# Optimization experiments

Hardware: AMD Instinct MI355X
Metric: run time of the kernel (lower is better)

The kernel has to match this reference:

```python
import jax, jax.numpy as jnp
import numpy as np

EPSILON = 5.0
B, D, C = 262144, 512, 1000


def setup_inputs() -> dict:
    key = jax.random.key(0)
    k1, k2, k3 = jax.random.split(key, 3)
    features = jax.random.normal(k1, (B, D), dtype=jnp.float32)
    means = jax.random.normal(k2, (C, D), dtype=jnp.float32)
    labels = jax.random.randint(k3, (B,), 0, C, dtype=jnp.int64)
    return {"features": features, "means": means, "labels": labels}


def reference(features, means, labels):
    # Gather per-sample class mean: [B, D]
    gathered = means[labels]
    diff = features - gathered
    # Per-sample L2 distance, then hinge clamp(epsilon - dist, min=0), mean over batch
    dist = jnp.sqrt(jnp.sum(diff * diff, axis=-1))  # [B]
    loss = jnp.mean(jnp.maximum(EPSILON - dist, 0.0))
    return loss
```

## Files before the change

### kernel.cpp

```cpp
#include <hip/hip_runtime.h>

#define EPSILON 5.0f

constexpr int D = 512;
constexpr int BLOCKS = 2048;
constexpr int THREADS = 256;

__global__ __launch_bounds__(THREADS) void ncl_partial_kernel(
    const float* __restrict__ features,
    const float* __restrict__ means,
    const int* __restrict__ labels,
    float* __restrict__ partials,
    int B)
{
    const int lane  = threadIdx.x & 63;
    const int wave  = threadIdx.x >> 6;
    const int wavesPerBlock = THREADS >> 6;
    const int globalWave = blockIdx.x * wavesPerBlock + wave;
    const int totalWaves = gridDim.x * wavesPerBlock;

    float wsum = 0.0f;

    for (int row = globalWave; row < B; row += totalWaves) {
        const int cls = labels[row];
        const float4* f = reinterpret_cast<const float4*>(features + (size_t)row * D);
        const float4* m = reinterpret_cast<const float4*>(means    + (size_t)cls * D);

        float acc = 0.0f;
        #pragma unroll
        for (int k = 0; k < 2; ++k) {
            const float4 fv = f[lane + 64 * k];
            const float4 mv = m[lane + 64 * k];
            const float dx = fv.x - mv.x;
            const float dy = fv.y - mv.y;
            const float dz = fv.z - mv.z;
            const float dw = fv.w - mv.w;
            acc = fmaf(dx, dx, fmaf(dy, dy, fmaf(dz, dz, fmaf(dw, dw, acc))));
        }

        #pragma unroll
        for (int off = 32; off > 0; off >>= 1)
            acc += __shfl_xor(acc, off, 64);

        if (lane == 0) {
            const float dist = sqrtf(acc);
            wsum += fmaxf(EPSILON - dist, 0.0f);
        }
    }

    __shared__ float s[4];
    if (lane == 0) s[wave] = wsum;
    __syncthreads();
    if (threadIdx.x == 0) {
        float t = 0.0f;
        #pragma unroll
        for (int i = 0; i < wavesPerBlock; ++i) t += s[i];
        partials[blockIdx.x] = t;
    }
}

__global__ __launch_bounds__(THREADS) void ncl_final_kernel(
    const float* __restrict__ partials,
    int n,
    float* __restrict__ out,
    float invB)
{
    float t = 0.0f;
    for (int i = threadIdx.x; i < n; i += THREADS) t += partials[i];

    #pragma unroll
    for (int off = 32; off > 0; off >>= 1)
        t += __shfl_xor(t, off, 64);

    __shared__ float s[4];
    const int lane = threadIdx.x & 63;
    const int wave = threadIdx.x >> 6;
    if (lane == 0) s[wave] = t;
    __syncthreads();
    if (threadIdx.x == 0) {
        out[0] = (s[0] + s[1] + s[2] + s[3]) * invB;
    }
}

extern "C" void kernel_launch(void* const* d_in, const int* in_sizes, int n_in,
                              void* d_out, int out_size, void* d_ws, size_t ws_size,
                              hipStream_t stream) {
    const float* features = (const float*)d_in[0];
    const float* means    = (const float*)d_in[1];
    const int*   labels   = (const int*)d_in[2];
    float* out = (float*)d_out;

    const int B = in_sizes[2];
    float* partials = (float*)d_ws;

    ncl_partial_kernel<<<BLOCKS, THREADS, 0, stream>>>(features, means, labels,
                                                       partials, B);
    ncl_final_kernel<<<1, THREADS, 0, stream>>>(partials, BLOCKS, out,
                                                1.0f / (float)B);
}
```

Measured before the change: 112.4 us.

## Process four rows per wave with 16-lane groups and prefetch next labels

Each wave now handles four rows at once, with a 16-lane group per row. Each lane issues 8 float4 loads per row instead of 2, and the shuffle reduction shrinks to 4 steps. The label for the next iteration is prefetched one step ahead so the dependent means gather is not serialized behind the label load. The aim is more memory-level parallelism per wave in this bandwidth-bound kernel. The cost is a longer per-lane unroll, higher register use, and an extra wave-wide reduction of wsum at the end.

```diff
diff --git a/kernel.cpp b/kernel.cpp
--- a/kernel.cpp
+++ b/kernel.cpp
@@ -2,8 +2,7 @@
 
 #define EPSILON 5.0f
 
-constexpr int D = 512;
-constexpr int BLOCKS = 2048;
+constexpr int BLOCKS  = 2048;
 constexpr int THREADS = 256;
 
 __global__ __launch_bounds__(THREADS) void ncl_partial_kernel(
@@ -13,48 +12,65 @@
     float* __restrict__ partials,
     int B)
 {
-    const int lane  = threadIdx.x & 63;
-    const int wave  = threadIdx.x >> 6;
-    const int wavesPerBlock = THREADS >> 6;
-    const int globalWave = blockIdx.x * wavesPerBlock + wave;
-    const int totalWaves = gridDim.x * wavesPerBlock;
+    const int lane = threadIdx.x & 63;
+    const int sub  = lane & 15;
+    const int g    = lane >> 4;
+    const int globalWave = blockIdx.x * (THREADS >> 6) + (threadIdx.x >> 6);
+    const int totalWaves = gridDim.x * (THREADS >> 6);
+    const int nQuads = (B + 3) >> 2;
 
     float wsum = 0.0f;
 
-    for (int row = globalWave; row < B; row += totalWaves) {
-        const int cls = labels[row];
-        const float4* f = reinterpret_cast<const float4*>(features + (size_t)row * D);
-        const float4* m = reinterpret_cast<const float4*>(means    + (size_t)cls * D);
+    int q   = globalWave;
+    int row = q * 4 + g;
+    int cls = (q < nQuads && row < B) ? labels[row] : 0;
+
+    for (; q < nQuads; q += totalWaves) {
+        row = q * 4 + g;
+        const bool valid = (row < B);
+
+        const int nq   = q + totalWaves;
+        const int nrow = nq * 4 + g;
+        const int ncls = (nq < nQuads && nrow < B) ? labels[nrow] : 0;
 
         float acc = 0.0f;
-        #pragma unroll
-        for (int k = 0; k < 2; ++k) {
-            const float4 fv = f[lane + 64 * k];
-            const float4 mv = m[lane + 64 * k];
-            const float dx = fv.x - mv.x;
-            const float dy = fv.y - mv.y;
-            const float dz = fv.z - mv.z;
-            const float dw = fv.w - mv.w;
-            acc = fmaf(dx, dx, fmaf(dy, dy, fmaf(dz, dz, fmaf(dw, dw, acc))));
+        if (valid) {
+            const float4* f = reinterpret_cast<const float4*>(features) + (size_t)row * 128;
+            const float4* m = reinterpret_cast<const float4*>(means)    + (size_t)cls * 128;
+            #pragma unroll
+            for (int k = 0; k < 8; ++k) {
+                const float4 fv = f[sub + 16 * k];
+                const float4 mv = m[sub + 16 * k];
+                const float dx = fv.x - mv.x;
+                const float dy = fv.y - mv.y;
+                const float dz = fv.z - mv.z;
+                const float dw = fv.w - mv.w;
+                acc = fmaf(dx, dx, fmaf(dy, dy, fmaf(dz, dz, fmaf(dw, dw, acc))));
+            }
         }
 
         #pragma unroll
-        for (int off = 32; off > 0; off >>= 1)
+        for (int off = 8; off > 0; off >>= 1)
             acc += __shfl_xor(acc, off, 64);
 
-        if (lane == 0) {
-            const float dist = sqrtf(acc);
-            wsum += fmaxf(EPSILON - dist, 0.0f);
-        }
+        if (sub == 0 && valid)
+            wsum += fmaxf(EPSILON - sqrtf(acc), 0.0f);
+
+        cls = ncls;
     }
 
-    __shared__ float s[4];
-    if (lane == 0) s[wave] = wsum;
+    #pragma unroll
+    for (int off = 32; off > 0; off >>= 1)
+        wsum += __shfl_xor(wsum, off, 64);
+
+    __shared__ float s[THREADS >> 6];
+    const int wv = threadIdx.x >> 6;
+    if (lane == 0) s[wv] = wsum;
     __syncthreads();
     if (threadIdx.x == 0) {
         float t = 0.0f;
         #pragma unroll
-        for (int i = 0; i < wavesPerBlock; ++i) t += s[i];
+        for (int i = 0; i < (THREADS >> 6); ++i) t += s[i];
         partials[blockIdx.x] = t;
     }
 }
@@ -72,13 +88,16 @@
     for (int off = 32; off > 0; off >>= 1)
         t += __shfl_xor(t, off, 64);
 
-    __shared__ float s[4];
+    __shared__ float s[THREADS >> 6];
     const int lane = threadIdx.x & 63;
-    const int wave = threadIdx.x >> 6;
-    if (lane == 0) s[wave] = t;
+    const int wv   = threadIdx.x >> 6;
+    if (lane == 0) s[wv] = t;
     __syncthreads();
     if (threadIdx.x == 0) {
-        out[0] = (s[0] + s[1] + s[2] + s[3]) * invB;
+        float acc = 0.0f;
+        #pragma unroll
+        for (int i = 0; i < (THREADS >> 6); ++i) acc += s[i];
+        out[0] = acc * invB;
     }
 }
 
```

New measurement: 114.3 us. About the same (+1.7%).
